# Optimization experiments

Measured on AMD Instinct MI355X. Metric: run time of the kernel, lower is better.

The kernel has to match this reference:

```python
import jax, jax.numpy as jnp
import numpy as np

D = 128      # embed_dim
H = 8        # num_heads
HD = D // H  # head_dim
TANH_CLIP = 10.0
B, N = 256, 2000


def setup_inputs() -> dict:
    key = jax.random.key(0)
    ks = jax.random.split(key, 16)
    node_embedding = jax.random.normal(ks[0], (B, N, D), jnp.float32)
    graph_embed = jax.random.normal(ks[1], (B, D), jnp.float32)
    h_last = jax.random.normal(ks[2], (B, D), jnp.float32)
    h_first = jax.random.normal(ks[3], (B, D), jnp.float32)
    visited_mask = jax.random.randint(ks[4], (B, N), 0, 2) > 0
    visited_mask = visited_mask.at[:, 0].set(False)  # keep >=1 valid key per row
    s = 1.0 / np.sqrt(D)
    v_l = jax.random.normal(ks[5], (1, D), jnp.float32)
    v_f = jax.random.normal(ks[6], (1, D), jnp.float32)
    w_q = jax.random.uniform(ks[7], (D, 3 * D), jnp.float32, -s, s)   # Linear(3D->D) weight [out,in]
    w_k = jax.random.uniform(ks[8], (D, D), jnp.float32, -s, s)
    w_v = jax.random.uniform(ks[9], (D, D), jnp.float32, -s, s)
    in_proj_w = jax.random.uniform(ks[10], (3 * D, D), jnp.float32, -s, s)  # MHA packed qkv proj
    in_proj_b = jnp.zeros((3 * D,), jnp.float32)
    out_w = jax.random.uniform(ks[11], (D, D), jnp.float32, -s, s)    # MHA out_proj weight
    out_b = jnp.zeros((D,), jnp.float32)
    return {
        'node_embedding': node_embedding, 'graph_embed': graph_embed,
        'h_last': h_last, 'h_first': h_first, 'visited_mask': visited_mask, 't': 1,
        'v_l': v_l, 'v_f': v_f, 'w_q': w_q, 'w_k': w_k, 'w_v': w_v,
        'in_proj_w': in_proj_w, 'in_proj_b': in_proj_b, 'out_w': out_w, 'out_b': out_b,
    }


def reference(node_embedding, graph_embed, h_last, h_first, visited_mask, t,
              v_l, v_f, w_q, w_k, w_v, in_proj_w, in_proj_b, out_w, out_b):
    b, n, d = node_embedding.shape
    if t == 0:  # static python int
        h_last = jnp.broadcast_to(v_l, (b, d))
        h_first = jnp.broadcast_to(v_f, (b, d))
    context = jnp.concatenate([graph_embed, h_last, h_first], axis=-1)  # [B,3D]

    q0 = context @ w_q.T                        # [B,D]
    k0 = jnp.einsum('bnd,ed->bne', node_embedding, w_k)  # [B,N,D]
    v0 = jnp.einsum('bnd,ed->bne', node_embedding, w_v)

    # nn.MultiheadAttention internal projections (packed in_proj)
    wq_i, wk_i, wv_i = in_proj_w[:d], in_proj_w[d:2 * d], in_proj_w[2 * d:]
    bq, bk, bv = in_proj_b[:d], in_proj_b[d:2 * d], in_proj_b[2 * d:]
    qp = (q0 @ wq_i.T + bq).reshape(b, H, HD)                 # single query
    kp = (jnp.einsum('bnd,ed->bne', k0, wk_i) + bk).reshape(b, n, H, HD)
    vp = (jnp.einsum('bnd,ed->bne', v0, wv_i) + bv).reshape(b, n, H, HD)

    scores = jnp.einsum('bhe,bnhe->bhn', qp, kp) / np.sqrt(HD)  # [B,H,N]
    scores = jnp.where(visited_mask[:, None, :], -jnp.inf, scores)
    attn = jax.nn.softmax(scores, axis=-1)
    ctx = jnp.einsum('bhn,bnhe->bhe', attn, vp).reshape(b, d)
    h_c_new = ctx @ out_w.T + out_b                           # [B,D]

    logits = jnp.einsum('bd,bnd->bn', h_c_new, k0) / np.sqrt(d)
    logits = TANH_CLIP * jnp.tanh(logits)
    logits = jnp.where(visited_mask, -jnp.inf, logits)
    probs = jax.nn.softmax(logits, axis=-1)
    return probs, logits
```

## Files before the change

kernel.cpp:

```cpp
#include <hip/hip_runtime.h>
#include <math.h>

#define DD 128
#define HH 8
#define HDIM 16
#define BB 256
#define NNODES 2000
#define NSLICE 4
#define SLICE_LEN 500
#define TILE 32
#define NTILES 16
#define ROWPAD 132
#define QHPAD 160
#define TANH_CLIPF 10.0f
#define NEG_BIG -1e30f

#define WS_WKP   0
#define WS_WVP   16384
#define WS_QH    32768
#define WS_QB    294912
#define WS_PM    296960
#define WS_PS    305152
#define WS_PACC  313344
#define WS_G     1361920

__global__ void prep_weights(const float* __restrict__ w_k, const float* __restrict__ w_v,
                             const float* __restrict__ in_proj_w, float* __restrict__ ws) {
    int idx = blockIdx.x * 256 + threadIdx.x;
    int mat = idx >> 14;
    int e = (idx >> 7) & 127;
    int d = idx & 127;
    const float* A  = in_proj_w + (mat ? 2 * DD * DD : DD * DD) + e * DD;
    const float* Bm = mat ? w_v : w_k;
    float acc = 0.f;
    for (int c = 0; c < DD; ++c) acc += A[c] * Bm[c * DD + d];
    ws[(mat ? WS_WVP : WS_WKP) + e * DD + d] = acc;
}

__global__ void prep_query(const float* __restrict__ graph_embed, const float* __restrict__ h_last,
                           const float* __restrict__ h_first, const int* __restrict__ t_ptr,
                           const float* __restrict__ v_l, const float* __restrict__ v_f,
                           const float* __restrict__ w_q, const float* __restrict__ in_proj_w,
                           const float* __restrict__ in_proj_b, float* __restrict__ ws) {
    __shared__ float ctx[3 * DD];
    __shared__ float q0[DD];
    __shared__ float qp[DD];
    int b = blockIdx.x, t = threadIdx.x;
    int t0 = t_ptr[0];
    for (int j = t; j < 3 * DD; j += 128) {
        float v;
        if (j < DD)           v = graph_embed[b * DD + j];
        else if (j < 2 * DD)  v = (t0 == 0) ? v_l[j - DD]     : h_last[b * DD + j - DD];
        else                  v = (t0 == 0) ? v_f[j - 2 * DD] : h_first[b * DD + j - 2 * DD];
        ctx[j] = v;
    }
    __syncthreads();
    {
        float a = 0.f;
        const float* wr = w_q + (size_t)t * 3 * DD;
        for (int j = 0; j < 3 * DD; ++j) a += ctx[j] * wr[j];
        q0[t] = a;
    }
    __syncthreads();
    {
        float a = in_proj_b[t];
        const float* wr = in_proj_w + (size_t)t * DD;
        for (int c = 0; c < DD; ++c) a += q0[c] * wr[c];
        qp[t] = a;
    }
    __syncthreads();
    const float inv = 0.25f;
    float* Qh = ws + WS_QH + (size_t)b * (HH * DD);
    for (int h = 0; h < HH; ++h) {
        float a = 0.f;
        for (int e = 0; e < HDIM; ++e) a += qp[h * HDIM + e] * ws[WS_WKP + (h * HDIM + e) * DD + t];
        Qh[h * DD + t] = a * inv;
    }
    if (t < HH) {
        float a = 0.f;
        for (int e = 0; e < HDIM; ++e) a += qp[t * HDIM + e] * in_proj_b[DD + t * HDIM + e];
        ws[WS_QB + b * HH + t] = a * inv;
    }
}

__global__ __launch_bounds__(256, 4) void attn_pass(const float* __restrict__ node,
                                                    const int* __restrict__ visited,
                                                    float* __restrict__ ws) {
    __shared__ float tile[2][TILE * ROWPAD];
    __shared__ float qh_l[HH * QHPAD];
    __shared__ float p_l[HH * 33];
    __shared__ float qb_l[HH];
    __shared__ float m_l[HH], s_l[HH], sc_l[HH];
    __shared__ int   vis_l[TILE];

    int b = blockIdx.y, sl = blockIdx.x;
    int t = threadIdx.x;
    int n0 = sl * SLICE_LEN;

    for (int i = t; i < HH * DD; i += 256) {
        int h = i >> 7, d = i & 127;
        qh_l[h * QHPAD + 20 * (d >> 4) + (d & 15)] = ws[WS_QH + (size_t)b * (HH * DD) + i];
    }
    if (t < HH) { qb_l[t] = ws[WS_QB + b * HH + t]; m_l[t] = NEG_BIG; s_l[t] = 0.f; }

    const int h_a = t & 7, q_a = t >> 3;
    const int n_s = t >> 3, g_s = t & 7;
    float4 acc = make_float4(0.f, 0.f, 0.f, 0.f);
    float4 st[4];

    {
        for (int j = 0; j < 4; ++j) {
            int v = t + 256 * j;
            int row = v >> 5, c4 = v & 31;
            int n = n0 + row;
            int nc = n < NNODES ? n : NNODES - 1;
            st[j] = *(const float4*)(node + ((size_t)b * NNODES + nc) * DD + 4 * c4);
        }
    }

    for (int T = 0; T < NTILES; ++T) {
        int buf = T & 1;
        for (int j = 0; j < 4; ++j) {
            int v = t + 256 * j;
            int row = v >> 5, c4 = v & 31;
            *(float4*)(tile[buf] + row * ROWPAD + 4 * c4) = st[j];
        }
        if (t < TILE) {
            int n = n0 + T * TILE + t;
            vis_l[t] = (n < n0 + SLICE_LEN) ? visited[(size_t)b * NNODES + n] : 1;
        }
        if (T + 1 < NTILES) {
            for (int j = 0; j < 4; ++j) {
                int v = t + 256 * j;
                int row = v >> 5, c4 = v & 31;
                int n = n0 + (T + 1) * TILE + row;
                int nc = n < NNODES ? n : NNODES - 1;
                st[j] = *(const float4*)(node + ((size_t)b * NNODES + nc) * DD + 4 * c4);
            }
        }
        __syncthreads();

        float part[HH];
        for (int h = 0; h < HH; ++h) part[h] = 0.f;
        const float* rowp = tile[buf] + n_s * ROWPAD + 16 * g_s;
        const float* qbase = qh_l + 20 * g_s;
        for (int j = 0; j < 4; ++j) {
            float4 nd = *(const float4*)(rowp + 4 * j);
            for (int h = 0; h < HH; ++h) {
                float4 qv = *(const float4*)(qbase + h * QHPAD + 4 * j);
                part[h] += nd.x * qv.x + nd.y * qv.y + nd.z * qv.z + nd.w * qv.w;
            }
        }
        for (int m = 1; m <= 4; m <<= 1)
            for (int h = 0; h < HH; ++h)
                part[h] += __shfl_xor(part[h], m, 64);
        p_l[g_s * 33 + n_s] = vis_l[n_s] ? NEG_BIG : (part[g_s] + qb_l[g_s]);
        __syncthreads();

        if (t < 64) {
            int h = t >> 3, i = t & 7;
            float v0 = p_l[h * 33 + 4 * i + 0];
            float v1 = p_l[h * 33 + 4 * i + 1];
            float v2 = p_l[h * 33 + 4 * i + 2];
            float v3 = p_l[h * 33 + 4 * i + 3];
            float mx = fmaxf(fmaxf(v0, v1), fmaxf(v2, v3));
            for (int m = 1; m <= 4; m <<= 1) mx = fmaxf(mx, __shfl_xor(mx, m, 64));
            float m_old = m_l[h];
            float m_new = fmaxf(m_old, mx);
            float p0 = v0 > -1e29f ? expf(v0 - m_new) : 0.f;
            float p1 = v1 > -1e29f ? expf(v1 - m_new) : 0.f;
            float p2 = v2 > -1e29f ? expf(v2 - m_new) : 0.f;
            float p3 = v3 > -1e29f ? expf(v3 - m_new) : 0.f;
            float ps = p0 + p1 + p2 + p3;
            for (int m = 1; m <= 4; m <<= 1) ps += __shfl_xor(ps, m, 64);
            p_l[h * 33 + 4 * i + 0] = p0;
            p_l[h * 33 + 4 * i + 1] = p1;
            p_l[h * 33 + 4 * i + 2] = p2;
            p_l[h * 33 + 4 * i + 3] = p3;
            if (i == 0) {
                float scale = expf(m_old - m_new);
                sc_l[h] = scale;
                m_l[h] = m_new;
                s_l[h] = s_l[h] * scale + ps;
            }
        }
        __syncthreads();

        float scale = sc_l[h_a];
        acc.x *= scale; acc.y *= scale; acc.z *= scale; acc.w *= scale;
        const float* tb = tile[buf];
        const float* pp = p_l + h_a * 33;
        for (int n = 0; n < TILE; ++n) {
            float p = pp[n];
            float4 nd = *(const float4*)(tb + n * ROWPAD + 4 * q_a);
            acc.x += p * nd.x; acc.y += p * nd.y; acc.z += p * nd.z; acc.w += p * nd.w;
        }
    }

    int slice_idx = b * NSLICE + sl;
    *(float4*)(ws + WS_PACC + (size_t)slice_idx * (HH * DD) + h_a * DD + 4 * q_a) = acc;
    if (t < HH) {
        ws[WS_PM + slice_idx * HH + t] = m_l[t];
        ws[WS_PS + slice_idx * HH + t] = s_l[t];
    }
}

__global__ void merge_kernel(const float* __restrict__ in_proj_b, const float* __restrict__ out_w,
                             const float* __restrict__ out_b, const float* __restrict__ w_k,
                             float* __restrict__ ws) {
    __shared__ float cn[HH][132];
    __shared__ float ctxv[DD];
    __shared__ float hc[DD];
    __shared__ float Mh[HH], Sh[HH];
    int b = blockIdx.x, t = threadIdx.x;
    if (t < HH) {
        float M = NEG_BIG;
        for (int i = 0; i < NSLICE; ++i) M = fmaxf(M, ws[WS_PM + (b * NSLICE + i) * HH + t]);
        float stot = 0.f;
        for (int i = 0; i < NSLICE; ++i) {
            float s = ws[WS_PS + (b * NSLICE + i) * HH + t];
            float m = ws[WS_PM + (b * NSLICE + i) * HH + t];
            stot += (s > 0.f) ? expf(m - M) * s : 0.f;
        }
        Mh[t] = M; Sh[t] = stot;
    }
    __syncthreads();
    for (int h = 0; h < HH; ++h) {
        float a = 0.f;
        for (int i = 0; i < NSLICE; ++i) {
            float m = ws[WS_PM + (b * NSLICE + i) * HH + h];
            float s = ws[WS_PS + (b * NSLICE + i) * HH + h];
            float w = (s > 0.f) ? expf(m - Mh[h]) : 0.f;
            a += w * ws[WS_PACC + (size_t)(b * NSLICE + i) * (HH * DD) + h * DD + t];
        }
        cn[h][t] = a / Sh[h];
    }
    __syncthreads();
    {
        int h = t >> 4;
        float a = in_proj_b[2 * DD + t];
        const float* wv = ws + WS_WVP + (size_t)t * DD;
        for (int d = 0; d < DD; ++d) a += cn[h][d] * wv[d];
        ctxv[t] = a;
    }
    __syncthreads();
    {
        float a = out_b[t];
        const float* wr = out_w + (size_t)t * DD;
        for (int c = 0; c < DD; ++c) a += ctxv[c] * wr[c];
        hc[t] = a;
    }
    __syncthreads();
    {
        const float invd = 0.08838834764831845f;
        float a = 0.f;
        for (int e = 0; e < DD; ++e) a += hc[e] * w_k[e * DD + t];
        ws[WS_G + b * DD + t] = a * invd;
    }
}

__global__ __launch_bounds__(1024, 1) void logits_pass(const float* __restrict__ node,
                                                       const int* __restrict__ visited,
                                                       const float* __restrict__ ws,
                                                       float* __restrict__ out) {
    __shared__ float gl[DD];
    __shared__ float ll[2048];
    __shared__ float red[16];
    int b = blockIdx.x, t = threadIdx.x;
    if (t < DD) gl[t] = ws[WS_G + b * DD + t];
    __syncthreads();
    int n_loc = t >> 3, g8 = t & 7;
    for (int r = 0; r < 16; ++r) {
        int n = r * 128 + n_loc;
        float a = 0.f;
        if (n < NNODES) {
            const float* rp = node + ((size_t)b * NNODES + n) * DD + g8 * 16;
            const float* gp = gl + g8 * 16;
            for (int j = 0; j < 4; ++j) {
                float4 nd = *(const float4*)(rp + 4 * j);
                float4 gv = *(const float4*)(gp + 4 * j);
                a += nd.x * gv.x + nd.y * gv.y + nd.z * gv.z + nd.w * gv.w;
            }
        }
        a += __shfl_xor(a, 1, 64);
        a += __shfl_xor(a, 2, 64);
        a += __shfl_xor(a, 4, 64);
        if (g8 == 0) {
            float v;
            if (n >= NNODES || visited[(size_t)b * NNODES + n]) v = NEG_BIG;
            else v = TANH_CLIPF * tanhf(a);
            ll[n] = v;
        }
    }
    __syncthreads();
    float mx = fmaxf(ll[t], ll[t + 1024]);
    for (int m = 1; m <= 32; m <<= 1) mx = fmaxf(mx, __shfl_xor(mx, m, 64));
    if ((t & 63) == 0) red[t >> 6] = mx;
    __syncthreads();
    if (t < 16) {
        float v = red[t];
        for (int m = 1; m <= 8; m <<= 1) v = fmaxf(v, __shfl_xor(v, m, 64));
        if (t == 0) red[0] = v;
    }
    __syncthreads();
    float M = red[0];
    __syncthreads();
    float e0 = expf(ll[t] - M), e1 = expf(ll[t + 1024] - M);
    float sm = e0 + e1;
    for (int m = 1; m <= 32; m <<= 1) sm += __shfl_xor(sm, m, 64);
    if ((t & 63) == 0) red[t >> 6] = sm;
    __syncthreads();
    if (t < 16) {
        float v = red[t];
        for (int m = 1; m <= 8; m <<= 1) v += __shfl_xor(v, m, 64);
        if (t == 0) red[0] = v;
    }
    __syncthreads();
    float inv = 1.0f / red[0];
    size_t pbase = (size_t)b * NNODES;
    size_t lbase = (size_t)BB * NNODES + pbase;
    if (t < NNODES)        { out[pbase + t] = e0 * inv;          out[lbase + t] = ll[t]; }
    if (t + 1024 < NNODES) { out[pbase + t + 1024] = e1 * inv;   out[lbase + t + 1024] = ll[t + 1024]; }
}

extern "C" void kernel_launch(void* const* d_in, const int* in_sizes, int n_in,
                              void* d_out, int out_size, void* d_ws, size_t ws_size,
                              hipStream_t stream) {
    const float* node        = (const float*)d_in[0];
    const float* graph_embed = (const float*)d_in[1];
    const float* h_last      = (const float*)d_in[2];
    const float* h_first     = (const float*)d_in[3];
    const int*   visited     = (const int*)d_in[4];
    const int*   t_ptr       = (const int*)d_in[5];
    const float* v_l         = (const float*)d_in[6];
    const float* v_f         = (const float*)d_in[7];
    const float* w_q         = (const float*)d_in[8];
    const float* w_k         = (const float*)d_in[9];
    const float* w_v         = (const float*)d_in[10];
    const float* in_proj_w   = (const float*)d_in[11];
    const float* in_proj_b   = (const float*)d_in[12];
    const float* out_w       = (const float*)d_in[13];
    const float* out_b       = (const float*)d_in[14];
    float* out = (float*)d_out;
    float* ws  = (float*)d_ws;

    prep_weights<<<128, 256, 0, stream>>>(w_k, w_v, in_proj_w, ws);
    prep_query<<<BB, 128, 0, stream>>>(graph_embed, h_last, h_first, t_ptr, v_l, v_f,
                                       w_q, in_proj_w, in_proj_b, ws);
    attn_pass<<<dim3(NSLICE, BB), 256, 0, stream>>>(node, visited, ws);
    merge_kernel<<<BB, 128, 0, stream>>>(in_proj_b, out_w, out_b, w_k, ws);
    logits_pass<<<BB, 1024, 0, stream>>>(node, visited, ws, out);
}
```

Measured before the change: 506.6 us.

## Restructure attention to per-wave slices and split logits into parallel dot plus softmax

The attention pass now gives each wavefront its own 125-node slice (16 slices per batch) with a private swizzled LDS chunk buffer. Scores, online softmax and accumulation all happen with wave shuffles, so block-wide barriers are gone. The logits pass is split into a highly parallel dot/tanh kernel that writes logits to workspace and a separate softmax kernel, replacing the single 1024-thread block per batch. This aims to raise parallelism and remove sync overhead, at the cost of more partial results to merge and an extra workspace round-trip for the logits.

```diff
diff --git a/kernel.cpp b/kernel.cpp
--- a/kernel.cpp
+++ b/kernel.cpp
@@ -3,15 +3,12 @@
 
 #define DD 128
 #define HH 8
-#define HDIM 16
 #define BB 256
 #define NNODES 2000
-#define NSLICE 4
-#define SLICE_LEN 500
-#define TILE 32
-#define NTILES 16
-#define ROWPAD 132
-#define QHPAD 160
+#define NSL 16
+#define SLEN 125
+#define CH 8
+#define NCH 16
 #define TANH_CLIPF 10.0f
 #define NEG_BIG -1e30f
 
@@ -20,9 +17,10 @@
 #define WS_QH    32768
 #define WS_QB    294912
 #define WS_PM    296960
-#define WS_PS    305152
-#define WS_PACC  313344
-#define WS_G     1361920
+#define WS_PS    329728
+#define WS_PACC  362496
+#define WS_G     4556800
+#define WS_LL    4589568
 
 __global__ void prep_weights(const float* __restrict__ w_k, const float* __restrict__ w_v,
                              const float* __restrict__ in_proj_w, float* __restrict__ ws) {
@@ -73,12 +71,12 @@
     float* Qh = ws + WS_QH + (size_t)b * (HH * DD);
     for (int h = 0; h < HH; ++h) {
         float a = 0.f;
-        for (int e = 0; e < HDIM; ++e) a += qp[h * HDIM + e] * ws[WS_WKP + (h * HDIM + e) * DD + t];
+        for (int e = 0; e < 16; ++e) a += qp[h * 16 + e] * ws[WS_WKP + (h * 16 + e) * DD + t];
         Qh[h * DD + t] = a * inv;
     }
     if (t < HH) {
         float a = 0.f;
-        for (int e = 0; e < HDIM; ++e) a += qp[t * HDIM + e] * in_proj_b[DD + t * HDIM + e];
+        for (int e = 0; e < 16; ++e) a += qp[t * 16 + e] * in_proj_b[DD + t * 16 + e];
         ws[WS_QB + b * HH + t] = a * inv;
     }
 }
@@ -86,122 +84,152 @@
 __global__ __launch_bounds__(256, 4) void attn_pass(const float* __restrict__ node,
                                                     const int* __restrict__ visited,
                                                     float* __restrict__ ws) {
-    __shared__ float tile[2][TILE * ROWPAD];
-    __shared__ float qh_l[HH * QHPAD];
-    __shared__ float p_l[HH * 33];
-    __shared__ float qb_l[HH];
-    __shared__ float m_l[HH], s_l[HH], sc_l[HH];
-    __shared__ int   vis_l[TILE];
-
-    int b = blockIdx.y, sl = blockIdx.x;
-    int t = threadIdx.x;
-    int n0 = sl * SLICE_LEN;
-
-    for (int i = t; i < HH * DD; i += 256) {
-        int h = i >> 7, d = i & 127;
-        qh_l[h * QHPAD + 20 * (d >> 4) + (d & 15)] = ws[WS_QH + (size_t)b * (HH * DD) + i];
-    }
-    if (t < HH) { qb_l[t] = ws[WS_QB + b * HH + t]; m_l[t] = NEG_BIG; s_l[t] = 0.f; }
-
-    const int h_a = t & 7, q_a = t >> 3;
-    const int n_s = t >> 3, g_s = t & 7;
-    float4 acc = make_float4(0.f, 0.f, 0.f, 0.f);
-    float4 st[4];
-
-    {
-        for (int j = 0; j < 4; ++j) {
-            int v = t + 256 * j;
-            int row = v >> 5, c4 = v & 31;
-            int n = n0 + row;
-            int nc = n < NNODES ? n : NNODES - 1;
-            st[j] = *(const float4*)(node + ((size_t)b * NNODES + nc) * DD + 4 * c4);
-        }
-    }
-
-    for (int T = 0; T < NTILES; ++T) {
-        int buf = T & 1;
-        for (int j = 0; j < 4; ++j) {
-            int v = t + 256 * j;
-            int row = v >> 5, c4 = v & 31;
-            *(float4*)(tile[buf] + row * ROWPAD + 4 * c4) = st[j];
-        }
-        if (t < TILE) {
-            int n = n0 + T * TILE + t;
-            vis_l[t] = (n < n0 + SLICE_LEN) ? visited[(size_t)b * NNODES + n] : 1;
-        }
-        if (T + 1 < NTILES) {
-            for (int j = 0; j < 4; ++j) {
-                int v = t + 256 * j;
-                int row = v >> 5, c4 = v & 31;
-                int n = n0 + (T + 1) * TILE + row;
-                int nc = n < NNODES ? n : NNODES - 1;
-                st[j] = *(const float4*)(node + ((size_t)b * NNODES + nc) * DD + 4 * c4);
-            }
-        }
-        __syncthreads();
-
-        float part[HH];
-        for (int h = 0; h < HH; ++h) part[h] = 0.f;
-        const float* rowp = tile[buf] + n_s * ROWPAD + 16 * g_s;
-        const float* qbase = qh_l + 20 * g_s;
-        for (int j = 0; j < 4; ++j) {
-            float4 nd = *(const float4*)(rowp + 4 * j);
-            for (int h = 0; h < HH; ++h) {
-                float4 qv = *(const float4*)(qbase + h * QHPAD + 4 * j);
-                part[h] += nd.x * qv.x + nd.y * qv.y + nd.z * qv.z + nd.w * qv.w;
-            }
-        }
-        for (int m = 1; m <= 4; m <<= 1)
-            for (int h = 0; h < HH; ++h)
-                part[h] += __shfl_xor(part[h], m, 64);
-        p_l[g_s * 33 + n_s] = vis_l[n_s] ? NEG_BIG : (part[g_s] + qb_l[g_s]);
-        __syncthreads();
-
-        if (t < 64) {
-            int h = t >> 3, i = t & 7;
-            float v0 = p_l[h * 33 + 4 * i + 0];
-            float v1 = p_l[h * 33 + 4 * i + 1];
-            float v2 = p_l[h * 33 + 4 * i + 2];
-            float v3 = p_l[h * 33 + 4 * i + 3];
-            float mx = fmaxf(fmaxf(v0, v1), fmaxf(v2, v3));
-            for (int m = 1; m <= 4; m <<= 1) mx = fmaxf(mx, __shfl_xor(mx, m, 64));
-            float m_old = m_l[h];
-            float m_new = fmaxf(m_old, mx);
-            float p0 = v0 > -1e29f ? expf(v0 - m_new) : 0.f;
-            float p1 = v1 > -1e29f ? expf(v1 - m_new) : 0.f;
-            float p2 = v2 > -1e29f ? expf(v2 - m_new) : 0.f;
-            float p3 = v3 > -1e29f ? expf(v3 - m_new) : 0.f;
-            float ps = p0 + p1 + p2 + p3;
-            for (int m = 1; m <= 4; m <<= 1) ps += __shfl_xor(ps, m, 64);
-            p_l[h * 33 + 4 * i + 0] = p0;
-            p_l[h * 33 + 4 * i + 1] = p1;
-            p_l[h * 33 + 4 * i + 2] = p2;
-            p_l[h * 33 + 4 * i + 3] = p3;
-            if (i == 0) {
-                float scale = expf(m_old - m_new);
-                sc_l[h] = scale;
-                m_l[h] = m_new;
-                s_l[h] = s_l[h] * scale + ps;
-            }
-        }
-        __syncthreads();
-
-        float scale = sc_l[h_a];
-        acc.x *= scale; acc.y *= scale; acc.z *= scale; acc.w *= scale;
-        const float* tb = tile[buf];
-        const float* pp = p_l + h_a * 33;
-        for (int n = 0; n < TILE; ++n) {
-            float p = pp[n];
-            float4 nd = *(const float4*)(tb + n * ROWPAD + 4 * q_a);
-            acc.x += p * nd.x; acc.y += p * nd.y; acc.z += p * nd.z; acc.w += p * nd.w;
-        }
-    }
-
-    int slice_idx = b * NSLICE + sl;
-    *(float4*)(ws + WS_PACC + (size_t)slice_idx * (HH * DD) + h_a * DD + 4 * q_a) = acc;
-    if (t < HH) {
-        ws[WS_PM + slice_idx * HH + t] = m_l[t];
-        ws[WS_PS + slice_idx * HH + t] = s_l[t];
+    __shared__ float lds[4][CH * DD];
+    int b    = blockIdx.x >> 2;
+    int wq   = blockIdx.x & 3;
+    int wave = threadIdx.x >> 6;
+    int lane = threadIdx.x & 63;
+    int sl   = wq * 4 + wave;
+    int n0   = sl * SLEN;
+    int c = lane >> 3, h = lane & 7;
+    float* buf = lds[wave];
+
+    const float* nb = node + (size_t)b * NNODES * DD;
+
+    float4 qf0, qf1, qf2, qf3;
+    {
+        const float* qp = ws + WS_QH + (size_t)b * (HH * DD) + h * DD + c * 16;
+        qf0 = *(const float4*)(qp + 0);
+        qf1 = *(const float4*)(qp + 4);
+        qf2 = *(const float4*)(qp + 8);
+        qf3 = *(const float4*)(qp + 12);
+    }
+    float qb = ws[WS_QB + b * HH + h];
+
+    const int* vb = visited + (size_t)b * NNODES;
+    int vis0 = vb[n0 + (lane < SLEN ? lane : SLEN - 1)];
+    int vis1 = vb[n0 + (lane + 64 < SLEN ? lane + 64 : SLEN - 1)];
+
+    const int rsw0 = ((0 ^ ((c >> 1) & 3)) << 2);
+    const int rsw1 = ((1 ^ ((c >> 1) & 3)) << 2);
+    const int rsw2 = ((2 ^ ((c >> 1) & 3)) << 2);
+    const int rsw3 = ((3 ^ ((c >> 1) & 3)) << 2);
+    const int rbase = c * 16;
+
+    const int srow = lane >> 3, scw = lane & 7;
+    const int wb = srow * DD + scw * 16;
+    const int wsw0 = ((0 ^ ((scw >> 1) & 3)) << 2);
+    const int wsw1 = ((1 ^ ((scw >> 1) & 3)) << 2);
+    const int wsw2 = ((2 ^ ((scw >> 1) & 3)) << 2);
+    const int wsw3 = ((3 ^ ((scw >> 1) & 3)) << 2);
+
+    float4 st0, st1, st2, st3;
+    {
+        int n = n0 + srow; if (n > NNODES - 1) n = NNODES - 1;
+        const float* p = nb + (size_t)n * DD + scw * 16;
+        st0 = *(const float4*)(p + 0); st1 = *(const float4*)(p + 4);
+        st2 = *(const float4*)(p + 8); st3 = *(const float4*)(p + 12);
+    }
+
+    float m_h = NEG_BIG, s_h = 0.f;
+    float4 a0 = make_float4(0.f,0.f,0.f,0.f), a1 = a0, a2 = a0, a3 = a0;
+
+    for (int i = 0; i < NCH; ++i) {
+        *(float4*)(buf + wb + wsw0) = st0;
+        *(float4*)(buf + wb + wsw1) = st1;
+        *(float4*)(buf + wb + wsw2) = st2;
+        *(float4*)(buf + wb + wsw3) = st3;
+        if (i + 1 < NCH) {
+            int n = n0 + (i + 1) * CH + srow; if (n > NNODES - 1) n = NNODES - 1;
+            const float* p = nb + (size_t)n * DD + scw * 16;
+            st0 = *(const float4*)(p + 0); st1 = *(const float4*)(p + 4);
+            st2 = *(const float4*)(p + 8); st3 = *(const float4*)(p + 12);
+        }
+        asm volatile("s_waitcnt lgkmcnt(0)" ::: "memory");
+        __builtin_amdgcn_sched_barrier(0);
+
+#define SCORE_N(n, dst) { \
+            const float* rp = buf + (n) * DD + rbase; \
+            float4 f0 = *(const float4*)(rp + rsw0); \
+            float4 f1 = *(const float4*)(rp + rsw1); \
+            float4 f2 = *(const float4*)(rp + rsw2); \
+            float4 f3 = *(const float4*)(rp + rsw3); \
+            dst = f0.x*qf0.x + f0.y*qf0.y + f0.z*qf0.z + f0.w*qf0.w \
+                + f1.x*qf1.x + f1.y*qf1.y + f1.z*qf1.z + f1.w*qf1.w \
+                + f2.x*qf2.x + f2.y*qf2.y + f2.z*qf2.z + f2.w*qf2.w \
+                + f3.x*qf3.x + f3.y*qf3.y + f3.z*qf3.z + f3.w*qf3.w; }
+        float v0,v1,v2,v3,v4,v5,v6,v7;
+        SCORE_N(0, v0) SCORE_N(1, v1) SCORE_N(2, v2) SCORE_N(3, v3)
+        SCORE_N(4, v4) SCORE_N(5, v5) SCORE_N(6, v6) SCORE_N(7, v7)
+#undef SCORE_N
+
+        float t0 = __shfl_xor(v0, 8, 64), t1 = __shfl_xor(v1, 8, 64);
+        float t2 = __shfl_xor(v2, 8, 64), t3 = __shfl_xor(v3, 8, 64);
+        float t4 = __shfl_xor(v4, 8, 64), t5 = __shfl_xor(v5, 8, 64);
+        float t6 = __shfl_xor(v6, 8, 64), t7 = __shfl_xor(v7, 8, 64);
+        int ck = c & 1;
+        float u0 = ck ? (v1 + t1) : (v0 + t0);
+        float u1 = ck ? (v3 + t3) : (v2 + t2);
+        float u2 = ck ? (v5 + t5) : (v4 + t4);
+        float u3 = ck ? (v7 + t7) : (v6 + t6);
+        float s0 = __shfl_xor(u0, 16, 64), s1 = __shfl_xor(u1, 16, 64);
+        float s2 = __shfl_xor(u2, 16, 64), s3 = __shfl_xor(u3, 16, 64);
+        ck = (c >> 1) & 1;
+        float w0 = ck ? (u1 + s1) : (u0 + s0);
+        float w1 = ck ? (u3 + s3) : (u2 + s2);
+        float r0 = __shfl_xor(w0, 32, 64), r1 = __shfl_xor(w1, 32, 64);
+        ck = (c >> 2) & 1;
+        float dotv = ck ? (w1 + r1) : (w0 + r0);
+
+        int nidx = i * CH + c;
+        int vlow  = __shfl(vis0, nidx & 63, 64);
+        int vhigh = __shfl(vis1, nidx & 63, 64);
+        int vv = (nidx < 64) ? vlow : vhigh;
+        bool maskd = (nidx >= SLEN) || (vv != 0);
+        float sc = maskd ? NEG_BIG : (dotv + qb);
+
+        float mx = sc;
+        mx = fmaxf(mx, __shfl_xor(mx, 8, 64));
+        mx = fmaxf(mx, __shfl_xor(mx, 16, 64));
+        mx = fmaxf(mx, __shfl_xor(mx, 32, 64));
+        float m_new = fmaxf(m_h, mx);
+        float p = (sc <= -1e29f) ? 0.f : expf(sc - m_new);
+        float ps = p;
+        ps += __shfl_xor(ps, 8, 64);
+        ps += __shfl_xor(ps, 16, 64);
+        ps += __shfl_xor(ps, 32, 64);
+        float scale = expf(m_h - m_new);
+        s_h = s_h * scale + ps;
+        m_h = m_new;
+        a0.x *= scale; a0.y *= scale; a0.z *= scale; a0.w *= scale;
+        a1.x *= scale; a1.y *= scale; a1.z *= scale; a1.w *= scale;
+        a2.x *= scale; a2.y *= scale; a2.z *= scale; a2.w *= scale;
+        a3.x *= scale; a3.y *= scale; a3.z *= scale; a3.w *= scale;
+
+#pragma unroll
+        for (int n = 0; n < CH; ++n) {
+            float pn = __shfl(p, n * 8 + h, 64);
+            const float* rp = buf + n * DD + rbase;
+            float4 f0 = *(const float4*)(rp + rsw0);
+            float4 f1 = *(const float4*)(rp + rsw1);
+            float4 f2 = *(const float4*)(rp + rsw2);
+            float4 f3 = *(const float4*)(rp + rsw3);
+            a0.x += pn * f0.x; a0.y += pn * f0.y; a0.z += pn * f0.z; a0.w += pn * f0.w;
+            a1.x += pn * f1.x; a1.y += pn * f1.y; a1.z += pn * f1.z; a1.w += pn * f1.w;
+            a2.x += pn * f2.x; a2.y += pn * f2.y; a2.z += pn * f2.z; a2.w += pn * f2.w;
+            a3.x += pn * f3.x; a3.y += pn * f3.y; a3.z += pn * f3.z; a3.w += pn * f3.w;
+        }
+        __builtin_amdgcn_sched_barrier(0);
+    }
+
+    size_t pb = WS_PACC + (size_t)((b * NSL + sl) * HH + h) * DD + c * 16;
+    *(float4*)(ws + pb + 0)  = a0;
+    *(float4*)(ws + pb + 4)  = a1;
+    *(float4*)(ws + pb + 8)  = a2;
+    *(float4*)(ws + pb + 12) = a3;
+    if (c == 0) {
+        ws[WS_PM + (b * NSL + sl) * HH + h] = m_h;
+        ws[WS_PS + (b * NSL + sl) * HH + h] = s_h;
     }
 }
 
@@ -215,11 +243,11 @@
     int b = blockIdx.x, t = threadIdx.x;
     if (t < HH) {
         float M = NEG_BIG;
-        for (int i = 0; i < NSLICE; ++i) M = fmaxf(M, ws[WS_PM + (b * NSLICE + i) * HH + t]);
+        for (int i = 0; i < NSL; ++i) M = fmaxf(M, ws[WS_PM + (b * NSL + i) * HH + t]);
         float stot = 0.f;
-        for (int i = 0; i < NSLICE; ++i) {
-            float s = ws[WS_PS + (b * NSLICE + i) * HH + t];
-            float m = ws[WS_PM + (b * NSLICE + i) * HH + t];
+        for (int i = 0; i < NSL; ++i) {
+            float s = ws[WS_PS + (b * NSL + i) * HH + t];
+            float m = ws[WS_PM + (b * NSL + i) * HH + t];
             stot += (s > 0.f) ? expf(m - M) * s : 0.f;
         }
         Mh[t] = M; Sh[t] = stot;
@@ -227,11 +255,11 @@
     __syncthreads();
     for (int h = 0; h < HH; ++h) {
         float a = 0.f;
-        for (int i = 0; i < NSLICE; ++i) {
-            float m = ws[WS_PM + (b * NSLICE + i) * HH + h];
-            float s = ws[WS_PS + (b * NSLICE + i) * HH + h];
+        for (int i = 0; i < NSL; ++i) {
+            float m = ws[WS_PM + (b * NSL + i) * HH + h];
+            float s = ws[WS_PS + (b * NSL + i) * HH + h];
             float w = (s > 0.f) ? expf(m - Mh[h]) : 0.f;
-            a += w * ws[WS_PACC + (size_t)(b * NSLICE + i) * (HH * DD) + h * DD + t];
+            a += w * ws[WS_PACC + (size_t)((b * NSL + i) * HH + h) * DD + t];
         }
         cn[h][t] = a / Sh[h];
     }
@@ -259,68 +287,88 @@
     }
 }
 
-__global__ __launch_bounds__(1024, 1) void logits_pass(const float* __restrict__ node,
-                                                       const int* __restrict__ visited,
-                                                       const float* __restrict__ ws,
-                                                       float* __restrict__ out) {
-    __shared__ float gl[DD];
-    __shared__ float ll[2048];
-    __shared__ float red[16];
-    int b = blockIdx.x, t = threadIdx.x;
-    if (t < DD) gl[t] = ws[WS_G + b * DD + t];
-    __syncthreads();
-    int n_loc = t >> 3, g8 = t & 7;
-    for (int r = 0; r < 16; ++r) {
-        int n = r * 128 + n_loc;
-        float a = 0.f;
-        if (n < NNODES) {
-            const float* rp = node + ((size_t)b * NNODES + n) * DD + g8 * 16;
-            const float* gp = gl + g8 * 16;
-            for (int j = 0; j < 4; ++j) {
-                float4 nd = *(const float4*)(rp + 4 * j);
-                float4 gv = *(const float4*)(gp + 4 * j);
-                a += nd.x * gv.x + nd.y * gv.y + nd.z * gv.z + nd.w * gv.w;
-            }
-        }
+__global__ __launch_bounds__(256, 8) void logits_ll(const float* __restrict__ node,
+                                                    const int* __restrict__ visited,
+                                                    float* __restrict__ ws) {
+    int b = blockIdx.x >> 3, seg = blockIdx.x & 7;
+    int wave = threadIdx.x >> 6, lane = threadIdx.x & 63;
+    int r8 = lane >> 3, g = lane & 7;
+    int base = seg * 250;
+    const float* nb = node + (size_t)b * NNODES * DD;
+    float4 g0, g1, g2, g3;
+    {
+        const float* gp = ws + WS_G + b * DD + g * 16;
+        g0 = *(const float4*)(gp + 0); g1 = *(const float4*)(gp + 4);
+        g2 = *(const float4*)(gp + 8); g3 = *(const float4*)(gp + 12);
+    }
+    float4 c0, c1, c2, c3;
+    {
+        int n = base + wave * 8 + r8;
+        const float* p = nb + (size_t)n * DD + g * 16;
+        c0 = *(const float4*)(p + 0); c1 = *(const float4*)(p + 4);
+        c2 = *(const float4*)(p + 8); c3 = *(const float4*)(p + 12);
+    }
+    for (int it = 0; it < 8; ++it) {
+        int rl = it * 32 + wave * 8 + r8;
+        int row = base + rl;
+        float4 n0 = c0, n1 = c1, n2 = c2, n3 = c3;
+        if (it + 1 < 8) {
+            int nr = base + (it + 1) * 32 + wave * 8 + r8;
+            if (nr > NNODES - 1) nr = NNODES - 1;
+            const float* p = nb + (size_t)nr * DD + g * 16;
+            c0 = *(const float4*)(p + 0); c1 = *(const float4*)(p + 4);
+            c2 = *(const float4*)(p + 8); c3 = *(const float4*)(p + 12);
+        }
+        float a = n0.x*g0.x + n0.y*g0.y + n0.z*g0.z + n0.w*g0.w
+                + n1.x*g1.x + n1.y*g1.y + n1.z*g1.z + n1.w*g1.w
+                + n2.x*g2.x + n2.y*g2.y + n2.z*g2.z + n2.w*g2.w
+                + n3.x*g3.x + n3.y*g3.y + n3.z*g3.z + n3.w*g3.w;
         a += __shfl_xor(a, 1, 64);
         a += __shfl_xor(a, 2, 64);
         a += __shfl_xor(a, 4, 64);
-        if (g8 == 0) {
-            float v;
-            if (n >= NNODES || visited[(size_t)b * NNODES + n]) v = NEG_BIG;
-            else v = TANH_CLIPF * tanhf(a);
-            ll[n] = v;
-        }
-    }
-    __syncthreads();
-    float mx = fmaxf(ll[t], ll[t + 1024]);
+        float val = TANH_CLIPF * tanhf(a);
+        if (g == 0 && rl < 250) {
+            if (visited[(size_t)b * NNODES + row]) val = NEG_BIG;
+            ws[WS_LL + (size_t)b * NNODES + row] = val;
+        }
+    }
+}
+
+__global__ __launch_bounds__(256, 4) void softmax_out(const float* __restrict__ ws,
+                                                      float* __restrict__ out) {
+    __shared__ float red[4];
+    int b = blockIdx.x, t = threadIdx.x;
+    const float* ll = ws + WS_LL + (size_t)b * NNODES;
+    float v0[8];
+#pragma unroll
+    for (int j = 0; j < 8; ++j) {
+        int idx = j * 256 + t;
+        v0[j] = (idx < NNODES) ? ll[idx] : NEG_BIG;
+    }
+    float mx = v0[0];
+#pragma unroll
+    for (int j = 1; j < 8; ++j) mx = fmaxf(mx, v0[j]);
     for (int m = 1; m <= 32; m <<= 1) mx = fmaxf(mx, __shfl_xor(mx, m, 64));
-    if ((t & 63) == 0) red[t >> 6] = mx;
-    __syncthreads();
-    if (t < 16) {
-        float v = red[t];
-        for (int m = 1; m <= 8; m <<= 1) v = fmaxf(v, __shfl_xor(v, m, 64));
-        if (t == 0) red[0] = v;
-    }
-    __syncthreads();
-    float M = red[0];
-    __syncthreads();
-    float e0 = expf(ll[t] - M), e1 = expf(ll[t + 1024] - M);
-    float sm = e0 + e1;
+    int wv = t >> 6;
+    if ((t & 63) == 0) red[wv] = mx;
+    __syncthreads();
+    float M = fmaxf(fmaxf(red[0], red[1]), fmaxf(red[2], red[3]));
+    __syncthreads();
+    float e[8]; float sm = 0.f;
+#pragma unroll
+    for (int j = 0; j < 8; ++j) { e[j] = expf(v0[j] - M); sm += e[j]; }
     for (int m = 1; m <= 32; m <<= 1) sm += __shfl_xor(sm, m, 64);
-    if ((t & 63) == 0) red[t >> 6] = sm;
-    __syncthreads();
-    if (t < 16) {
-        float v = red[t];
-        for (int m = 1; m <= 8; m <<= 1) v += __shfl_xor(v, m, 64);
-        if (t == 0) red[0] = v;
-    }
-    __syncthreads();
-    float inv = 1.0f / red[0];
-    size_t pbase = (size_t)b * NNODES;
-    size_t lbase = (size_t)BB * NNODES + pbase;
-    if (t < NNODES)        { out[pbase + t] = e0 * inv;          out[lbase + t] = ll[t]; }
-    if (t + 1024 < NNODES) { out[pbase + t + 1024] = e1 * inv;   out[lbase + t + 1024] = ll[t + 1024]; }
+    if ((t & 63) == 0) red[wv] = sm;
+    __syncthreads();
+    float inv = 1.0f / (red[0] + red[1] + red[2] + red[3]);
+#pragma unroll
+    for (int j = 0; j < 8; ++j) {
+        int idx = j * 256 + t;
+        if (idx < NNODES) {
+            out[(size_t)b * NNODES + idx] = e[j] * inv;
+            out[(size_t)BB * NNODES + (size_t)b * NNODES + idx] = v0[j];
+        }
+    }
 }
 
 extern "C" void kernel_launch(void* const* d_in, const int* in_sizes, int n_in,
@@ -347,7 +395,8 @@
     prep_weights<<<128, 256, 0, stream>>>(w_k, w_v, in_proj_w, ws);
     prep_query<<<BB, 128, 0, stream>>>(graph_embed, h_last, h_first, t_ptr, v_l, v_f,
                                        w_q, in_proj_w, in_proj_b, ws);
-    attn_pass<<<dim3(NSLICE, BB), 256, 0, stream>>>(node, visited, ws);
+    attn_pass<<<BB * 4, 256, 0, stream>>>(node, visited, ws);
     merge_kernel<<<BB, 128, 0, stream>>>(in_proj_b, out_w, out_b, w_k, ws);
-    logits_pass<<<BB, 1024, 0, stream>>>(node, visited, ws, out);
-}
+    logits_ll<<<BB * 8, 256, 0, stream>>>(node, visited, ws);
+    softmax_out<<<BB, 256, 0, stream>>>(ws, out);
+}
```

After: 496.5 us. 2.0% less time.
